# Kernel tuning notes

Hardware: AMD Instinct MI355X
Metric: run time of the kernel (lower is better)

Reference implementation:

```python
import jax, jax.numpy as jnp
import numpy as np

V = 32000        # vocab_size
OOV = 100        # max_oovs
VT = V + OOV
E = 256          # embed_size
H = 256          # hidden_size
PAD_INDEX = 0


def _gru_cell(x, h, w_ih, w_hh, b_ih, b_hh):
    # PyTorch GRU gate order: r, z, n
    gi = x @ w_ih.T + b_ih
    gh = h @ w_hh.T + b_hh
    ir, iz, inn = jnp.split(gi, 3, axis=-1)
    hr, hz, hn = jnp.split(gh, 3, axis=-1)
    r = jax.nn.sigmoid(ir + hr)
    z = jax.nn.sigmoid(iz + hz)
    n = jnp.tanh(inn + r * hn)
    return (1.0 - z) * n + z * h


def setup_inputs() -> dict:
    key = jax.random.key(0)
    ks = jax.random.split(key, 16)
    bs, max_len, seq_len = 32, 64, 128
    inputs = jax.random.randint(ks[0], (bs, max_len), 0, V, dtype=jnp.int32)
    encoded = jax.random.normal(ks[1], (bs, seq_len, 2 * H), dtype=jnp.float32)
    encoded_idx = jax.random.randint(ks[2], (bs, seq_len), 0, VT, dtype=jnp.int32)
    s = 0.02
    return {
        "inputs": inputs,
        "encoded": encoded,
        "encoded_idx": encoded_idx,
        "bridge_w": s * jax.random.normal(ks[3], (H, 2 * H), dtype=jnp.float32),
        "embed": s * jax.random.normal(ks[4], (V, E), dtype=jnp.float32),
        "gru_w_ih": s * jax.random.normal(ks[5], (3 * H, E + 2 * H), dtype=jnp.float32),
        "gru_w_hh": s * jax.random.normal(ks[6], (3 * H, H), dtype=jnp.float32),
        "gru_b_ih": jnp.zeros((3 * H,), dtype=jnp.float32),
        "gru_b_hh": jnp.zeros((3 * H,), dtype=jnp.float32),
        "Wg_w": s * jax.random.normal(ks[7], (V, H), dtype=jnp.float32),
        "Wg_b": jnp.zeros((V,), dtype=jnp.float32),
        "Wo_w": s * jax.random.normal(ks[8], (H, 2 * H), dtype=jnp.float32),
        "Wo_b": jnp.zeros((H,), dtype=jnp.float32),
    }


def decoder_forward(inputs, encoded, encoded_idx, bridge_w, embed,
                    gru_w_ih, gru_w_hh, gru_b_ih, gru_b_hh,
                    Wg_w, Wg_b, Wo_w, Wo_b):
    bs, seq_len, _ = encoded.shape
    # precomputed per-sequence quantities (as in original forward())
    enc_scores = jnp.tanh(encoded @ Wo_w.T + Wo_b)            # [bs, seq, H]
    pad_mask = jnp.where(encoded_idx == PAD_INDEX, -1000.0, 0.0)  # [bs, seq]
    b_idx = jnp.arange(bs)[:, None]

    s0 = encoded[:, -1, :] @ bridge_w.T                        # [bs, H]
    ctx0 = jnp.zeros((bs, 2 * H), dtype=encoded.dtype)

    def step(carry, inp):
        s_prev, ctx = carry
        x = embed[inp]                                         # [bs, E]
        gru_in = jnp.concatenate([x, ctx], axis=-1)            # [bs, E+2H]
        s_t = _gru_cell(gru_in, s_prev, gru_w_ih, gru_w_hh, gru_b_ih, gru_b_hh)
        psi_g = s_t @ Wg_w.T + Wg_b                            # [bs, V]
        psi_c = jnp.einsum('bsh,bh->bs', enc_scores, s_t) + pad_mask
        p = jax.nn.softmax(jnp.concatenate([psi_g, psi_c], axis=1), axis=1)
        prob_g = jnp.concatenate(
            [p[:, :V], jnp.full((bs, OOV), 1e-4, dtype=p.dtype)], axis=1)  # [bs, VT]
        prob_c = p[:, V:]                                      # [bs, seq]
        # scatter-add of copy probs onto extended vocab (one-hot bmm in original)
        prob_c_to_g = jnp.zeros((bs, VT), dtype=p.dtype).at[b_idx, encoded_idx].add(prob_c)
        out = prob_g + prob_c_to_g                             # [bs, VT]
        # selective read: reweight copy probs at positions matching current input
        rel = (encoded_idx == inp[:, None]).astype(p.dtype)
        cw = rel * prob_c
        cw = cw / jnp.maximum(cw.sum(axis=1, keepdims=True), 1e-12)  # F.normalize p=1
        new_ctx = jnp.einsum('bs,bsd->bd', cw, encoded)        # [bs, 2H]
        return (s_t, new_ctx), out

    (_, _), outs = jax.lax.scan(step, (s0, ctx0), inputs.T)    # [max_len, bs, VT]
    return jnp.transpose(outs, (1, 0, 2))                      # [bs, max_len, VT]


def reference(inputs, encoded, encoded_idx, bridge_w, embed,
              gru_w_ih, gru_w_hh, gru_b_ih, gru_b_hh,
              Wg_w, Wg_b, Wo_w, Wo_b):
    return decoder_forward(inputs, encoded, encoded_idx, bridge_w, embed,
                           gru_w_ih, gru_w_hh, gru_b_ih, gru_b_hh,
                           Wg_w, Wg_b, Wo_w, Wo_b)
```

## Files before the change

kernel.cpp:

```cpp
#include <hip/hip_runtime.h>
#include <math.h>
#include <stdint.h>

static const int VOC  = 32000;
static const int VT_  = 32100;

typedef __attribute__((ext_vector_type(8))) short bf16x8_t;
typedef __attribute__((ext_vector_type(4))) float f32x4_t;

__device__ __forceinline__ unsigned short f2bf(float f) {
  union { float f; unsigned int u; } v; v.f = f;
  unsigned int u = v.u;
  u = u + 0x7FFFu + ((u >> 16) & 1u);
  return (unsigned short)(u >> 16);
}
__device__ __forceinline__ float bf2f(unsigned short u) {
  union { unsigned int i; float f; } w; w.i = ((unsigned int)u) << 16; return w.f;
}
__device__ __forceinline__ float bfbits(unsigned int u) {
  union { unsigned int i; float f; } w; w.i = u; return w.f;
}
__device__ __forceinline__ int nth_set(unsigned long long m0, unsigned long long m1, int j) {
  int c0 = __popcll(m0);
  unsigned long long m = m0; int base = 0;
  if (j >= c0) { j -= c0; m = m1; base = 64; }
  for (int k = 0; k < j; k++) m &= m - 1;
  return base + (__ffsll((long long)m) - 1);
}

__global__ __launch_bounds__(256) void k_pre(
    const float* __restrict__ wg, unsigned short* __restrict__ WG16,
    const float* __restrict__ whh, unsigned short* __restrict__ WHH16,
    const float* __restrict__ enc, const float* __restrict__ wo,
    const float* __restrict__ wob, float* __restrict__ ENCSC,
    const float* __restrict__ bridge, float* __restrict__ S0,
    const float* __restrict__ embed, const int* __restrict__ inputs,
    const float* __restrict__ wih, const float* __restrict__ bih, float* __restrict__ XG,
    const int* __restrict__ encidx, float* __restrict__ ENCIH) {
  __shared__ int flag;
  int q = blockIdx.x;
  int tid = threadIdx.x;
  if (q < 256) {
    int bm = q >> 2, bn = q & 3;
    int ti = tid & 15, tj = tid >> 4;
    int r0 = bm * 64 + ti * 4;
    int n0 = bn * 64 + tj * 4;
    const float4* A[4]; const float4* B[4];
#pragma unroll
    for (int i = 0; i < 4; i++) A[i] = (const float4*)(enc + (size_t)(r0 + i) * 512);
#pragma unroll
    for (int j = 0; j < 4; j++) B[j] = (const float4*)(wo + (size_t)(n0 + j) * 512);
    float acc[4][4];
#pragma unroll
    for (int i = 0; i < 4; i++)
#pragma unroll
      for (int j = 0; j < 4; j++) acc[i][j] = 0.f;
    for (int k = 0; k < 128; k++) {
      float4 a[4], b[4];
#pragma unroll
      for (int i = 0; i < 4; i++) a[i] = A[i][k];
#pragma unroll
      for (int j = 0; j < 4; j++) b[j] = B[j][k];
#pragma unroll
      for (int i = 0; i < 4; i++)
#pragma unroll
        for (int j = 0; j < 4; j++)
          acc[i][j] += a[i].x * b[j].x + a[i].y * b[j].y + a[i].z * b[j].z + a[i].w * b[j].w;
    }
#pragma unroll
    for (int i = 0; i < 4; i++)
#pragma unroll
      for (int j = 0; j < 4; j++)
        ENCSC[(size_t)(r0 + i) * 256 + n0 + j] = tanhf(acc[i][j] + wob[n0 + j]);
  } else if (q < 640) {
    int p = q - 256;
    int bm = p & 31, bn = p >> 5;
    int ti = tid & 15, tj = tid >> 4;
    int r0 = bm * 64 + ti * 4;
    int n0 = bn * 64 + tj * 4;
    const float4* A[4]; const float4* B[4];
#pragma unroll
    for (int i = 0; i < 4; i++) A[i] = (const float4*)(embed + (size_t)inputs[r0 + i] * 256);
#pragma unroll
    for (int j = 0; j < 4; j++) B[j] = (const float4*)(wih + (size_t)(n0 + j) * 768);
    float acc[4][4];
#pragma unroll
    for (int i = 0; i < 4; i++)
#pragma unroll
      for (int j = 0; j < 4; j++) acc[i][j] = 0.f;
    for (int k = 0; k < 64; k++) {
      float4 a[4], b[4];
#pragma unroll
      for (int i = 0; i < 4; i++) a[i] = A[i][k];
#pragma unroll
      for (int j = 0; j < 4; j++) b[j] = B[j][k];
#pragma unroll
      for (int i = 0; i < 4; i++)
#pragma unroll
        for (int j = 0; j < 4; j++)
          acc[i][j] += a[i].x * b[j].x + a[i].y * b[j].y + a[i].z * b[j].z + a[i].w * b[j].w;
    }
#pragma unroll
    for (int i = 0; i < 4; i++)
#pragma unroll
      for (int j = 0; j < 4; j++)
        XG[(size_t)(r0 + i) * 768 + n0 + j] = acc[i][j] + bih[n0 + j];
  } else if (q < 1664) {
    int n4 = 32000 * 256 / 4;
    for (int i = (q - 640) * 256 + tid; i < n4; i += 1024 * 256) {
      float4 f = ((const float4*)wg)[i];
      ushort4 o;
      o.x = f2bf(f.x); o.y = f2bf(f.y); o.z = f2bf(f.z); o.w = f2bf(f.w);
      ((ushort4*)WG16)[i] = o;
    }
  } else if (q < 1676) {
    int n4 = 768 * 256 / 4;
    for (int i = (q - 1664) * 256 + tid; i < n4; i += 12 * 256) {
      float4 f = ((const float4*)whh)[i];
      ushort4 o;
      o.x = f2bf(f.x); o.y = f2bf(f.y); o.z = f2bf(f.z); o.w = f2bf(f.w);
      ((ushort4*)WHH16)[i] = o;
    }
  } else if (q < 1708) {
    int b = q - 1676, h = tid;
    const float4* a4 = (const float4*)(enc + ((size_t)b * 128 + 127) * 512);
    const float4* w4 = (const float4*)(bridge + (size_t)h * 512);
    float acc = 0.f;
    for (int k = 0; k < 128; k++) {
      float4 a = a4[k], w = w4[k];
      acc += a.x * w.x + a.y * w.y + a.z * w.z + a.w * w.w;
    }
    S0[b * 256 + h] = acc;
  } else {
    int bs = q - 1708;
    int b = bs >> 7;
    int idx = encidx[bs];
    if (tid < 64) {
      unsigned long long m = __ballot(inputs[b * 64 + tid] == idx);
      if (tid == 0) flag = (m != 0ULL);
    }
    __syncthreads();
    if (!flag) return;
    const float4* e4 = (const float4*)(enc + (size_t)bs * 512);
    for (int d = tid; d < 768; d += 256) {
      const float4* w4 = (const float4*)(wih + (size_t)d * 768 + 256);
      float acc = 0.f;
      for (int k = 0; k < 128; k++) {
        float4 e = e4[k], w = w4[k];
        acc += e.x * w.x + e.y * w.y + e.z * w.z + e.w * w.w;
      }
      ENCIH[(size_t)bs * 768 + d] = acc;
    }
  }
}

__global__ __launch_bounds__(768, 1) void k_seq(
    const unsigned short* __restrict__ whb,
    const float* __restrict__ bhh,
    const float* __restrict__ xg, const float* __restrict__ encsc,
    const float* __restrict__ encih, const int* __restrict__ encidx,
    const int* __restrict__ inputs, const float* __restrict__ s0,
    float* __restrict__ S32, unsigned short* __restrict__ S16) {
  __shared__ float sbuf[256];
  __shared__ __align__(16) unsigned short sb16[256];
  __shared__ float ghp[768];
  __shared__ float psis[128];
  __shared__ int eidx_sh[128];
  __shared__ int inp_sh[64];
  __shared__ unsigned long long mmask[64][2];
  __shared__ __align__(16) unsigned short wlds[73728];
  int b = blockIdx.x;
  int tid = threadIdx.x;
  int wid = tid >> 6, lane = tid & 63;
  int quad = lane >> 4, l15 = lane & 15;
  int n0 = wid * 64;
  int h = tid;
#pragma unroll
  for (int c = 0; c < 4; c++)
#pragma unroll
    for (int kt2 = 0; kt2 < 3; kt2++) {
      int4 v = *(const int4*)(whb + (size_t)(n0 + c * 16 + l15) * 256 + 160 + kt2 * 32 + quad * 8);
      *(int4*)(wlds + wid * 6144 + (c * 3 + kt2) * 512 + (l15 * 4 + quad) * 8) = v;
    }
  bf16x8_t wf[20];
#pragma unroll
  for (int c = 0; c < 4; c++)
#pragma unroll
    for (int kt = 0; kt < 5; kt++)
      wf[c * 5 + kt] = *(const bf16x8_t*)(whb + (size_t)(n0 + c * 16 + l15) * 256 + kt * 32 + quad * 8);
  float bR = 0.f, bZ = 0.f, bN = 0.f, ctxR = 0.f, ctxZ = 0.f, ctxN = 0.f;
  if (tid < 256) {
    bR = bhh[h]; bZ = bhh[256 + h]; bN = bhh[512 + h];
    float v = s0[b * 256 + tid];
    sbuf[tid] = v;
    sb16[tid] = f2bf(v);
  }
  if (tid < 128) eidx_sh[tid] = encidx[b * 128 + tid];
  if (tid < 64) inp_sh[tid] = inputs[b * 64 + tid];
  __syncthreads();
  if (tid < 128) {
    int e = eidx_sh[tid];
    for (int t = 0; t < 64; t++) {
      unsigned long long bal = __ballot(e == inp_sh[t]);
      if (lane == 0) mmask[t][wid] = bal;
    }
  }
  __syncthreads();
  for (int t = 0; t < 64; t++) {
    int r = b * 64 + t;
    float xr0 = 0.f, xr1 = 0.f, xr2 = 0.f;
    if (tid < 256) {
      const float* xr = xg + (size_t)r * 768;
      xr0 = xr[h]; xr1 = xr[256 + h]; xr2 = xr[512 + h];
    }
    f32x4_t a0 = {0.f,0.f,0.f,0.f}, a1 = {0.f,0.f,0.f,0.f};
    f32x4_t a2 = {0.f,0.f,0.f,0.f}, a3 = {0.f,0.f,0.f,0.f};
#pragma unroll
    for (int kt = 0; kt < 5; kt++) {
      bf16x8_t af = *(const bf16x8_t*)(sb16 + kt * 32 + quad * 8);
      a0 = __builtin_amdgcn_mfma_f32_16x16x32_bf16(af, wf[ 0 + kt], a0, 0, 0, 0);
      a1 = __builtin_amdgcn_mfma_f32_16x16x32_bf16(af, wf[ 5 + kt], a1, 0, 0, 0);
      a2 = __builtin_amdgcn_mfma_f32_16x16x32_bf16(af, wf[10 + kt], a2, 0, 0, 0);
      a3 = __builtin_amdgcn_mfma_f32_16x16x32_bf16(af, wf[15 + kt], a3, 0, 0, 0);
    }
#pragma unroll
    for (int kt2 = 0; kt2 < 3; kt2++) {
      bf16x8_t af = *(const bf16x8_t*)(sb16 + (5 + kt2) * 32 + quad * 8);
      const unsigned short* wb = wlds + wid * 6144 + kt2 * 512 + (l15 * 4 + quad) * 8;
      a0 = __builtin_amdgcn_mfma_f32_16x16x32_bf16(af, *(const bf16x8_t*)(wb +    0), a0, 0, 0, 0);
      a1 = __builtin_amdgcn_mfma_f32_16x16x32_bf16(af, *(const bf16x8_t*)(wb + 1536), a1, 0, 0, 0);
      a2 = __builtin_amdgcn_mfma_f32_16x16x32_bf16(af, *(const bf16x8_t*)(wb + 3072), a2, 0, 0, 0);
      a3 = __builtin_amdgcn_mfma_f32_16x16x32_bf16(af, *(const bf16x8_t*)(wb + 4608), a3, 0, 0, 0);
    }
    if (lane < 16) {
      ghp[n0 +      lane] = a0[0];
      ghp[n0 + 16 + lane] = a1[0];
      ghp[n0 + 32 + lane] = a2[0];
      ghp[n0 + 48 + lane] = a3[0];
    }
    __syncthreads();
    if (tid < 256) {
      float hr = ghp[h] + bR;
      float hz = ghp[256 + h] + bZ;
      float hn = ghp[512 + h] + bN;
      float gr = xr0 + ctxR;
      float gz = xr1 + ctxZ;
      float gn = xr2 + ctxN;
      float rgate = 1.f / (1.f + expf(-(gr + hr)));
      float zgate = 1.f / (1.f + expf(-(gz + hz)));
      float ngate = tanhf(gn + rgate * hn);
      float sold = sbuf[h];
      float snew = (1.f - zgate) * ngate + zgate * sold;
      unsigned short u16 = f2bf(snew);
      S32[(size_t)r * 256 + h] = snew;
      S16[(size_t)r * 256 + h] = u16;
      sbuf[h] = snew;
      sb16[h] = u16;
    }
    __syncthreads();
    if (t == 63) break;
    unsigned long long m0 = mmask[t][0], m1 = mmask[t][1];
    int mc = __popcll(m0) + __popcll(m1);
    if (mc > 0) {
      for (int j = wid; j < mc; j += 12) {
        int s = nth_set(m0, m1, j);
        const float4* e4 = (const float4*)(encsc + (size_t)(b * 128 + s) * 256);
        float4 ev = e4[lane];
        float4 sv = ((const float4*)sbuf)[lane];
        float v = ev.x * sv.x + ev.y * sv.y + ev.z * sv.z + ev.w * sv.w;
#pragma unroll
        for (int off = 32; off >= 1; off >>= 1) v += __shfl_down(v, off);
        if (lane == 0) psis[j] = v + (eidx_sh[s] == 0 ? -1000.f : 0.f);
      }
      __syncthreads();
      if (tid == 0) {
        float mx = -3e38f;
        for (int j = 0; j < mc; j++) mx = fmaxf(mx, psis[j]);
        if (mx < -500.f) {
          for (int j = 0; j < mc; j++) psis[j] = 0.f;
        } else {
          float ss = 0.f;
          for (int j = 0; j < mc; j++) { float e = expf(psis[j] - mx); psis[j] = e; ss += e; }
          float rs = 1.f / ss;
          for (int j = 0; j < mc; j++) psis[j] *= rs;
        }
      }
      __syncthreads();
      if (tid < 256) {
        ctxR = 0.f; ctxZ = 0.f; ctxN = 0.f;
        unsigned long long mm0 = m0, mm1 = m1;
        for (int j = 0; j < mc; j++) {
          int s;
          if (mm0) { s = __ffsll((long long)mm0) - 1; mm0 &= mm0 - 1; }
          else     { s = 64 + __ffsll((long long)mm1) - 1; mm1 &= mm1 - 1; }
          float c = psis[j];
          const float* e = encih + (size_t)(b * 128 + s) * 768;
          ctxR += c * e[h]; ctxZ += c * e[256 + h]; ctxN += c * e[512 + h];
        }
      }
    } else if (tid < 256) {
      ctxR = 0.f; ctxZ = 0.f; ctxN = 0.f;
    }
  }
}

__global__ __launch_bounds__(256, 2) void k_mid(const unsigned short* __restrict__ S16,
                                                const unsigned short* __restrict__ WG16,
                                                const float* __restrict__ wgb,
                                                unsigned short* __restrict__ pe16,
                                                const float* __restrict__ S32,
                                                const float* __restrict__ encsc,
                                                const int* __restrict__ encidx,
                                                float* __restrict__ psic) {
  __shared__ unsigned short lA[2][128 * 64];
  __shared__ unsigned short lB[2][128 * 64];
  int q = blockIdx.x;
  int tid = threadIdx.x;
  if (q >= 4000) {
    int q2 = q - 4000;
    int b = q2 >> 1, ny = q2 & 1;
    int ti = tid & 15, tj = tid >> 4;
    int r0 = b * 64 + ti * 4;
    int s0 = ny * 64 + tj * 4;
    const float4* A[4]; const float4* B[4];
#pragma unroll
    for (int i = 0; i < 4; i++) A[i] = (const float4*)(S32 + (size_t)(r0 + i) * 256);
#pragma unroll
    for (int j = 0; j < 4; j++) B[j] = (const float4*)(encsc + (size_t)(b * 128 + s0 + j) * 256);
    float acc[4][4];
#pragma unroll
    for (int i = 0; i < 4; i++)
#pragma unroll
      for (int j = 0; j < 4; j++) acc[i][j] = 0.f;
    for (int k = 0; k < 64; k++) {
      float4 a[4], bb[4];
#pragma unroll
      for (int i = 0; i < 4; i++) a[i] = A[i][k];
#pragma unroll
      for (int j = 0; j < 4; j++) bb[j] = B[j][k];
#pragma unroll
      for (int i = 0; i < 4; i++)
#pragma unroll
        for (int j = 0; j < 4; j++)
          acc[i][j] += a[i].x * bb[j].x + a[i].y * bb[j].y + a[i].z * bb[j].z + a[i].w * bb[j].w;
    }
#pragma unroll
    for (int i = 0; i < 4; i++)
#pragma unroll
      for (int j = 0; j < 4; j++) {
        float v = acc[i][j] + (encidx[b * 128 + s0 + j] == 0 ? -1000.f : 0.f);
        psic[(size_t)(r0 + i) * 128 + s0 + j] = v;
      }
    return;
  }
  int nc = q % 250, mt = q / 250;
  int wid = tid >> 6, lane = tid & 63;
  int wm = wid >> 1, wn = wid & 1;
  int quad = lane >> 4, l15 = lane & 15;
  f32x4_t acc[4][4];
#pragma unroll
  for (int i = 0; i < 4; i++)
#pragma unroll
    for (int j = 0; j < 4; j++) acc[i][j] = (f32x4_t){0.f, 0.f, 0.f, 0.f};

#define STAGE_MID(buf, kt) do {                                                            \
    _Pragma("unroll")                                                                      \
    for (int u = 0; u < 4; u++) {                                                          \
      int c = u * 256 + tid;                                                               \
      int row = c >> 3;                                                                    \
      int ko = ((c & 7) ^ (row & 7)) * 8;                                                  \
      __builtin_amdgcn_global_load_lds(                                                    \
          (const __attribute__((address_space(1))) unsigned int*)(S16 + (size_t)(mt * 128 + row) * 256 + (kt) * 64 + ko), \
          (__attribute__((address_space(3))) unsigned int*)(&lA[buf][c * 8]), 16, 0, 0);   \
      __builtin_amdgcn_global_load_lds(                                                    \
          (const __attribute__((address_space(1))) unsigned int*)(WG16 + (size_t)(nc * 128 + row) * 256 + (kt) * 64 + ko), \
          (__attribute__((address_space(3))) unsigned int*)(&lB[buf][c * 8]), 16, 0, 0);   \
    }                                                                                      \
  } while (0)

  STAGE_MID(0, 0);
  __syncthreads();
  for (int kt = 0; kt < 4; kt++) {
    int cur = kt & 1;
    if (kt < 3) STAGE_MID(cur ^ 1, kt + 1);
#pragma unroll
    for (int ks = 0; ks < 2; ks++) {
      bf16x8_t af[4], bfr[4];
      int slot = ((ks * 4 + quad) ^ (l15 & 7)) * 8;
#pragma unroll
      for (int i = 0; i < 4; i++) af[i] = *(const bf16x8_t*)(&lA[cur][(wm * 64 + i * 16 + l15) * 64 + slot]);
#pragma unroll
      for (int j = 0; j < 4; j++) bfr[j] = *(const bf16x8_t*)(&lB[cur][(wn * 64 + j * 16 + l15) * 64 + slot]);
#pragma unroll
      for (int i = 0; i < 4; i++)
#pragma unroll
        for (int j = 0; j < 4; j++)
          acc[i][j] = __builtin_amdgcn_mfma_f32_16x16x32_bf16(af[i], bfr[j], acc[i][j], 0, 0, 0);
    }
    __syncthreads();
  }
#undef STAGE_MID
  float bj[4];
#pragma unroll
  for (int j = 0; j < 4; j++) bj[j] = wgb[nc * 128 + wn * 64 + j * 16 + l15];
#pragma unroll
  for (int i = 0; i < 4; i++) {
#pragma unroll
    for (int p = 0; p < 4; p++) {
      int rg = mt * 128 + wm * 64 + i * 16 + quad * 4 + p;
      size_t base = (size_t)rg * 32000 + nc * 128 + wn * 64 + l15;
#pragma unroll
      for (int j = 0; j < 4; j++)
        pe16[base + j * 16] = f2bf(expf(acc[i][j][p] + bj[j]));
    }
  }
}

__global__ __launch_bounds__(256) void k_pb(const unsigned short* __restrict__ pe16,
                                            const float* __restrict__ psic,
                                            const int* __restrict__ encidx,
                                            float* __restrict__ outp) {
  __shared__ float red[8];
  int r = blockIdx.x;
  int b = r >> 6;
  int tid = threadIdx.x;
  int wid = tid >> 6, lane = tid & 63;
  const unsigned short* prow = pe16 + (size_t)r * 32000;
  float* orow = outp + (size_t)r * VT_;
  int4 ev[16];
#pragma unroll
  for (int u = 0; u < 16; u++) {
    int c8 = u * 256 + tid;
    if (c8 < 4000) ev[u] = *(const int4*)(prow + c8 * 8);
    else ev[u] = (int4){0, 0, 0, 0};
  }
  float sumE = 0.f;
#pragma unroll
  for (int u = 0; u < 16; u++) {
    unsigned int xs0 = (unsigned int)ev[u].x, xs1 = (unsigned int)ev[u].y;
    unsigned int xs2 = (unsigned int)ev[u].z, xs3 = (unsigned int)ev[u].w;
    sumE += bfbits(xs0 << 16) + bfbits(xs0 & 0xffff0000u);
    sumE += bfbits(xs1 << 16) + bfbits(xs1 & 0xffff0000u);
    sumE += bfbits(xs2 << 16) + bfbits(xs2 & 0xffff0000u);
    sumE += bfbits(xs3 << 16) + bfbits(xs3 & 0xffff0000u);
  }
  float t = sumE;
#pragma unroll
  for (int off = 32; off >= 1; off >>= 1) t += __shfl_xor(t, off);
  if (lane == 0) red[wid] = t;
  float pc = (tid < 128) ? psic[(size_t)r * 128 + tid] : -3e38f;
  float mv = pc;
#pragma unroll
  for (int off = 32; off >= 1; off >>= 1) mv = fmaxf(mv, __shfl_xor(mv, off));
  if (lane == 0) red[4 + wid] = mv;
  __syncthreads();
  float sumEt = red[0] + red[1] + red[2] + red[3];
  float Mc = fmaxf(fmaxf(red[4], red[5]), fmaxf(red[6], red[7]));
  float D = fmaxf(Mc - 30.f, 0.f);
  float w = expf(-D);
  __syncthreads();
  float ec = (tid < 128) ? expf(pc - D) : 0.f;
  float zt = ec;
#pragma unroll
  for (int off = 32; off >= 1; off >>= 1) zt += __shfl_xor(zt, off);
  if (lane == 0) red[wid] = zt;
  __syncthreads();
  float Z = w * sumEt + (red[0] + red[1] + red[2] + red[3]);
  float gs = w / Z;
#pragma unroll 2
  for (int u = 0; u < 16; u++) {
    int c8 = u * 256 + tid;
    if (c8 < 4000) {
      int c0 = c8 * 8;
      unsigned int xs0 = (unsigned int)ev[u].x, xs1 = (unsigned int)ev[u].y;
      unsigned int xs2 = (unsigned int)ev[u].z, xs3 = (unsigned int)ev[u].w;
      float4 o0, o1;
      o0.x = bfbits(xs0 << 16) * gs;         o0.y = bfbits(xs0 & 0xffff0000u) * gs;
      o0.z = bfbits(xs1 << 16) * gs;         o0.w = bfbits(xs1 & 0xffff0000u) * gs;
      o1.x = bfbits(xs2 << 16) * gs;         o1.y = bfbits(xs2 & 0xffff0000u) * gs;
      o1.z = bfbits(xs3 << 16) * gs;         o1.w = bfbits(xs3 & 0xffff0000u) * gs;
      *(float4*)(orow + c0) = o0;
      *(float4*)(orow + c0 + 4) = o1;
    }
  }
  if (tid < 100) orow[32000 + tid] = 1e-4f;
  __syncthreads();
  if (tid < 128) {
    int idx = encidx[b * 128 + tid];
    atomicAdd(&orow[idx], ec / Z);
  }
}

extern "C" void kernel_launch(void* const* d_in, const int* in_sizes, int n_in,
                              void* d_out, int out_size, void* d_ws, size_t ws_size,
                              hipStream_t stream) {
  (void)in_sizes; (void)n_in; (void)out_size; (void)ws_size;
  const int*   inputs  = (const int*)d_in[0];
  const float* encoded = (const float*)d_in[1];
  const int*   encidx  = (const int*)d_in[2];
  const float* bridge  = (const float*)d_in[3];
  const float* embed   = (const float*)d_in[4];
  const float* wih     = (const float*)d_in[5];
  const float* whh     = (const float*)d_in[6];
  const float* bih     = (const float*)d_in[7];
  const float* bhh     = (const float*)d_in[8];
  const float* wg      = (const float*)d_in[9];
  const float* wgb     = (const float*)d_in[10];
  const float* wo      = (const float*)d_in[11];
  const float* wob     = (const float*)d_in[12];
  float* out = (float*)d_out;

  char* ws = (char*)d_ws;
  size_t off = 0;
  auto alloc = [&](size_t bytes) -> void* {
    void* p = ws + off;
    off += (bytes + 255) & ~(size_t)255;
    return p;
  };
  unsigned short* WG16  = (unsigned short*)alloc((size_t)32000 * 256 * 2);
  unsigned short* WHH16 = (unsigned short*)alloc((size_t)768 * 256 * 2);
  float* S32            = (float*)alloc((size_t)2048 * 256 * 4);
  unsigned short* S16   = (unsigned short*)alloc((size_t)2048 * 256 * 2);
  float* ENCSC          = (float*)alloc((size_t)4096 * 256 * 4);
  float* ENCIH          = (float*)alloc((size_t)4096 * 768 * 4);
  float* XG             = (float*)alloc((size_t)2048 * 768 * 4);
  float* S0             = (float*)alloc((size_t)32 * 256 * 4);
  float* PSIC           = (float*)alloc((size_t)2048 * 128 * 4);
  unsigned short* PE16  = (unsigned short*)alloc((size_t)2048 * 32000 * 2);

  k_pre<<<5804, 256, 0, stream>>>(wg, WG16, whh, WHH16, encoded, wo, wob, ENCSC,
                                  bridge, S0, embed, inputs, wih, bih, XG,
                                  encidx, ENCIH);
  k_seq<<<32, 768, 0, stream>>>(WHH16, bhh, XG, ENCSC, ENCIH, encidx, inputs, S0, S32, S16);
  k_mid<<<4064, 256, 0, stream>>>(S16, WG16, wgb, PE16, S32, ENCSC, encidx, PSIC);
  k_pb<<<2048, 256, 0, stream>>>(PE16, PSIC, encidx, out);
}
```

Baseline: 837.0 us.

## Move precompute GEMMs to MFMA and make logits GEMM keep Wg tile resident

Splits the precompute kernel in two: the first converts enc/Wo into bf16 hi/lo pairs, and W_ih and the gathered embeddings into bf16. The second runs the encoder-score and input-gate GEMMs on MFMA, using a split-bf16 three-product scheme to keep fp32-like accuracy for the tanh scores. The logits kernel now launches one block per 128-column Wg tile, keeps the full-K tile in LDS, and loops over all 16 row tiles. This removes repeated Wg reloads at the cost of far fewer blocks (250), 128KB of LDS per block, and no double buffering.

```diff
diff --git a/kernel.cpp b/kernel.cpp
--- a/kernel.cpp
+++ b/kernel.cpp
@@ -28,101 +28,166 @@
   return base + (__ffsll((long long)m) - 1);
 }
 
-__global__ __launch_bounds__(256) void k_pre(
+__global__ __launch_bounds__(256) void k_pre0(
     const float* __restrict__ wg, unsigned short* __restrict__ WG16,
     const float* __restrict__ whh, unsigned short* __restrict__ WHH16,
-    const float* __restrict__ enc, const float* __restrict__ wo,
-    const float* __restrict__ wob, float* __restrict__ ENCSC,
-    const float* __restrict__ bridge, float* __restrict__ S0,
+    const float* __restrict__ enc, unsigned short* __restrict__ EH,
+    unsigned short* __restrict__ EL,
+    const float* __restrict__ wo, unsigned short* __restrict__ WOH,
+    unsigned short* __restrict__ WOL,
+    const float* __restrict__ wih, unsigned short* __restrict__ WIH16,
     const float* __restrict__ embed, const int* __restrict__ inputs,
-    const float* __restrict__ wih, const float* __restrict__ bih, float* __restrict__ XG,
-    const int* __restrict__ encidx, float* __restrict__ ENCIH) {
-  __shared__ int flag;
-  int q = blockIdx.x;
-  int tid = threadIdx.x;
-  if (q < 256) {
-    int bm = q >> 2, bn = q & 3;
-    int ti = tid & 15, tj = tid >> 4;
-    int r0 = bm * 64 + ti * 4;
-    int n0 = bn * 64 + tj * 4;
-    const float4* A[4]; const float4* B[4];
-#pragma unroll
-    for (int i = 0; i < 4; i++) A[i] = (const float4*)(enc + (size_t)(r0 + i) * 512);
-#pragma unroll
-    for (int j = 0; j < 4; j++) B[j] = (const float4*)(wo + (size_t)(n0 + j) * 512);
-    float acc[4][4];
-#pragma unroll
-    for (int i = 0; i < 4; i++)
-#pragma unroll
-      for (int j = 0; j < 4; j++) acc[i][j] = 0.f;
-    for (int k = 0; k < 128; k++) {
-      float4 a[4], b[4];
-#pragma unroll
-      for (int i = 0; i < 4; i++) a[i] = A[i][k];
-#pragma unroll
-      for (int j = 0; j < 4; j++) b[j] = B[j][k];
-#pragma unroll
-      for (int i = 0; i < 4; i++)
-#pragma unroll
-        for (int j = 0; j < 4; j++)
-          acc[i][j] += a[i].x * b[j].x + a[i].y * b[j].y + a[i].z * b[j].z + a[i].w * b[j].w;
-    }
-#pragma unroll
-    for (int i = 0; i < 4; i++)
-#pragma unroll
-      for (int j = 0; j < 4; j++)
-        ENCSC[(size_t)(r0 + i) * 256 + n0 + j] = tanhf(acc[i][j] + wob[n0 + j]);
-  } else if (q < 640) {
-    int p = q - 256;
-    int bm = p & 31, bn = p >> 5;
-    int ti = tid & 15, tj = tid >> 4;
-    int r0 = bm * 64 + ti * 4;
-    int n0 = bn * 64 + tj * 4;
-    const float4* A[4]; const float4* B[4];
-#pragma unroll
-    for (int i = 0; i < 4; i++) A[i] = (const float4*)(embed + (size_t)inputs[r0 + i] * 256);
-#pragma unroll
-    for (int j = 0; j < 4; j++) B[j] = (const float4*)(wih + (size_t)(n0 + j) * 768);
-    float acc[4][4];
-#pragma unroll
-    for (int i = 0; i < 4; i++)
-#pragma unroll
-      for (int j = 0; j < 4; j++) acc[i][j] = 0.f;
-    for (int k = 0; k < 64; k++) {
-      float4 a[4], b[4];
-#pragma unroll
-      for (int i = 0; i < 4; i++) a[i] = A[i][k];
-#pragma unroll
-      for (int j = 0; j < 4; j++) b[j] = B[j][k];
-#pragma unroll
-      for (int i = 0; i < 4; i++)
-#pragma unroll
-        for (int j = 0; j < 4; j++)
-          acc[i][j] += a[i].x * b[j].x + a[i].y * b[j].y + a[i].z * b[j].z + a[i].w * b[j].w;
-    }
-#pragma unroll
-    for (int i = 0; i < 4; i++)
-#pragma unroll
-      for (int j = 0; j < 4; j++)
-        XG[(size_t)(r0 + i) * 768 + n0 + j] = acc[i][j] + bih[n0 + j];
-  } else if (q < 1664) {
-    int n4 = 32000 * 256 / 4;
-    for (int i = (q - 640) * 256 + tid; i < n4; i += 1024 * 256) {
+    unsigned short* __restrict__ X16) {
+  int q = blockIdx.x, tid = threadIdx.x;
+  if (q < 1024) {
+    for (int i = q * 256 + tid; i < 2048000; i += 1024 * 256) {
       float4 f = ((const float4*)wg)[i];
       ushort4 o;
       o.x = f2bf(f.x); o.y = f2bf(f.y); o.z = f2bf(f.z); o.w = f2bf(f.w);
       ((ushort4*)WG16)[i] = o;
     }
-  } else if (q < 1676) {
-    int n4 = 768 * 256 / 4;
-    for (int i = (q - 1664) * 256 + tid; i < n4; i += 12 * 256) {
+  } else if (q < 1036) {
+    for (int i = (q - 1024) * 256 + tid; i < 49152; i += 12 * 256) {
       float4 f = ((const float4*)whh)[i];
       ushort4 o;
       o.x = f2bf(f.x); o.y = f2bf(f.y); o.z = f2bf(f.z); o.w = f2bf(f.w);
       ((ushort4*)WHH16)[i] = o;
     }
-  } else if (q < 1708) {
-    int b = q - 1676, h = tid;
+  } else if (q < 1292) {
+    for (int i = (q - 1036) * 256 + tid; i < 524288; i += 256 * 256) {
+      float4 f = ((const float4*)enc)[i];
+      ushort4 h, l;
+      h.x = f2bf(f.x); l.x = f2bf(f.x - bf2f(h.x));
+      h.y = f2bf(f.y); l.y = f2bf(f.y - bf2f(h.y));
+      h.z = f2bf(f.z); l.z = f2bf(f.z - bf2f(h.z));
+      h.w = f2bf(f.w); l.w = f2bf(f.w - bf2f(h.w));
+      ((ushort4*)EH)[i] = h;
+      ((ushort4*)EL)[i] = l;
+    }
+  } else if (q < 1300) {
+    for (int i = (q - 1292) * 256 + tid; i < 32768; i += 8 * 256) {
+      float4 f = ((const float4*)wo)[i];
+      ushort4 h, l;
+      h.x = f2bf(f.x); l.x = f2bf(f.x - bf2f(h.x));
+      h.y = f2bf(f.y); l.y = f2bf(f.y - bf2f(h.y));
+      h.z = f2bf(f.z); l.z = f2bf(f.z - bf2f(h.z));
+      h.w = f2bf(f.w); l.w = f2bf(f.w - bf2f(h.w));
+      ((ushort4*)WOH)[i] = h;
+      ((ushort4*)WOL)[i] = l;
+    }
+  } else if (q < 1312) {
+    for (int g = (q - 1300) * 256 + tid; g < 49152; g += 12 * 256) {
+      int row = g >> 6, col = g & 63;
+      float4 f = ((const float4*)(wih + (size_t)row * 768))[col];
+      ushort4 o;
+      o.x = f2bf(f.x); o.y = f2bf(f.y); o.z = f2bf(f.z); o.w = f2bf(f.w);
+      ((ushort4*)X16)[0];
+      ((ushort4*)WIH16)[g] = o;
+    }
+  } else {
+    for (int g = (q - 1312) * 256 + tid; g < 131072; g += 128 * 256) {
+      int r = g >> 6, col = g & 63;
+      float4 f = ((const float4*)(embed + (size_t)inputs[r] * 256))[col];
+      ushort4 o;
+      o.x = f2bf(f.x); o.y = f2bf(f.y); o.z = f2bf(f.z); o.w = f2bf(f.w);
+      ((ushort4*)X16)[g] = o;
+    }
+  }
+}
+
+__global__ __launch_bounds__(256) void k_pre1(
+    const unsigned short* __restrict__ EH, const unsigned short* __restrict__ EL,
+    const unsigned short* __restrict__ WOH, const unsigned short* __restrict__ WOL,
+    const float* __restrict__ wob, float* __restrict__ ENCSC,
+    const unsigned short* __restrict__ X16, const unsigned short* __restrict__ WIH16,
+    const float* __restrict__ bih, float* __restrict__ XG,
+    const float* __restrict__ enc, const float* __restrict__ bridge,
+    float* __restrict__ S0,
+    const float* __restrict__ wih, const int* __restrict__ encidx,
+    const int* __restrict__ inputs, float* __restrict__ ENCIH) {
+  __shared__ int flag;
+  int q = blockIdx.x, tid = threadIdx.x;
+  int wid = tid >> 6, lane = tid & 63;
+  int wm = wid >> 1, wn = wid & 1;
+  int quad = lane >> 4, l15 = lane & 15;
+  if (q < 256) {
+    int bm = q >> 2, bn = q & 3;
+    int r0 = bm * 64 + wm * 32, n0 = bn * 64 + wn * 32;
+    f32x4_t acc[2][2];
+#pragma unroll
+    for (int i = 0; i < 2; i++)
+#pragma unroll
+      for (int j = 0; j < 2; j++) acc[i][j] = (f32x4_t){0.f, 0.f, 0.f, 0.f};
+    for (int kc = 0; kc < 16; kc++) {
+      int ko = kc * 32 + quad * 8;
+      bf16x8_t ah[2], al[2], bh[2], bl[2];
+#pragma unroll
+      for (int i = 0; i < 2; i++) {
+        size_t off = (size_t)(r0 + i * 16 + l15) * 512 + ko;
+        ah[i] = *(const bf16x8_t*)(EH + off);
+        al[i] = *(const bf16x8_t*)(EL + off);
+      }
+#pragma unroll
+      for (int j = 0; j < 2; j++) {
+        size_t off = (size_t)(n0 + j * 16 + l15) * 512 + ko;
+        bh[j] = *(const bf16x8_t*)(WOH + off);
+        bl[j] = *(const bf16x8_t*)(WOL + off);
+      }
+#pragma unroll
+      for (int i = 0; i < 2; i++)
+#pragma unroll
+        for (int j = 0; j < 2; j++) {
+          acc[i][j] = __builtin_amdgcn_mfma_f32_16x16x32_bf16(ah[i], bh[j], acc[i][j], 0, 0, 0);
+          acc[i][j] = __builtin_amdgcn_mfma_f32_16x16x32_bf16(ah[i], bl[j], acc[i][j], 0, 0, 0);
+          acc[i][j] = __builtin_amdgcn_mfma_f32_16x16x32_bf16(al[i], bh[j], acc[i][j], 0, 0, 0);
+        }
+    }
+#pragma unroll
+    for (int i = 0; i < 2; i++)
+#pragma unroll
+      for (int j = 0; j < 2; j++)
+#pragma unroll
+        for (int p = 0; p < 4; p++) {
+          int row = r0 + i * 16 + quad * 4 + p;
+          int col = n0 + j * 16 + l15;
+          ENCSC[(size_t)row * 256 + col] = tanhf(acc[i][j][p] + wob[col]);
+        }
+  } else if (q < 640) {
+    int p2 = q - 256;
+    int bm = p2 & 31, bn = p2 >> 5;
+    int r0 = bm * 64 + wm * 32, n0 = bn * 64 + wn * 32;
+    f32x4_t acc[2][2];
+#pragma unroll
+    for (int i = 0; i < 2; i++)
+#pragma unroll
+      for (int j = 0; j < 2; j++) acc[i][j] = (f32x4_t){0.f, 0.f, 0.f, 0.f};
+    for (int kc = 0; kc < 8; kc++) {
+      int ko = kc * 32 + quad * 8;
+      bf16x8_t a[2], b[2];
+#pragma unroll
+      for (int i = 0; i < 2; i++)
+        a[i] = *(const bf16x8_t*)(X16 + (size_t)(r0 + i * 16 + l15) * 256 + ko);
+#pragma unroll
+      for (int j = 0; j < 2; j++)
+        b[j] = *(const bf16x8_t*)(WIH16 + (size_t)(n0 + j * 16 + l15) * 256 + ko);
+#pragma unroll
+      for (int i = 0; i < 2; i++)
+#pragma unroll
+        for (int j = 0; j < 2; j++)
+          acc[i][j] = __builtin_amdgcn_mfma_f32_16x16x32_bf16(a[i], b[j], acc[i][j], 0, 0, 0);
+    }
+#pragma unroll
+    for (int i = 0; i < 2; i++)
+#pragma unroll
+      for (int j = 0; j < 2; j++)
+#pragma unroll
+        for (int p = 0; p < 4; p++) {
+          int row = r0 + i * 16 + quad * 4 + p;
+          int col = n0 + j * 16 + l15;
+          XG[(size_t)row * 768 + col] = acc[i][j][p] + bih[col];
+        }
+  } else if (q < 672) {
+    int b = q - 640, h = tid;
     const float4* a4 = (const float4*)(enc + ((size_t)b * 128 + 127) * 512);
     const float4* w4 = (const float4*)(bridge + (size_t)h * 512);
     float acc = 0.f;
@@ -132,7 +197,7 @@
     }
     S0[b * 256 + h] = acc;
   } else {
-    int bs = q - 1708;
+    int bs = q - 672;
     int b = bs >> 7;
     int idx = encidx[bs];
     if (tid < 64) {
@@ -304,20 +369,18 @@
   }
 }
 
-__global__ __launch_bounds__(256, 2) void k_mid(const unsigned short* __restrict__ S16,
-                                                const unsigned short* __restrict__ WG16,
-                                                const float* __restrict__ wgb,
-                                                unsigned short* __restrict__ pe16,
-                                                const float* __restrict__ S32,
-                                                const float* __restrict__ encsc,
-                                                const int* __restrict__ encidx,
-                                                float* __restrict__ psic) {
-  __shared__ unsigned short lA[2][128 * 64];
-  __shared__ unsigned short lB[2][128 * 64];
+__global__ __launch_bounds__(256) void k_mid(const unsigned short* __restrict__ S16,
+                                             const unsigned short* __restrict__ WG16,
+                                             const float* __restrict__ wgb,
+                                             unsigned short* __restrict__ pe16,
+                                             const float* __restrict__ S32,
+                                             const float* __restrict__ encsc,
+                                             const int* __restrict__ encidx,
+                                             float* __restrict__ psic) {
   int q = blockIdx.x;
   int tid = threadIdx.x;
-  if (q >= 4000) {
-    int q2 = q - 4000;
+  if (q >= 250) {
+    int q2 = q - 250;
     int b = q2 >> 1, ny = q2 & 1;
     int ti = tid & 15, tj = tid >> 4;
     int r0 = b * 64 + ti * 4;
@@ -353,66 +416,68 @@
       }
     return;
   }
-  int nc = q % 250, mt = q / 250;
+  __shared__ unsigned short lB[128 * 256];
+  __shared__ unsigned short lA[128 * 256];
+  int nc = q;
   int wid = tid >> 6, lane = tid & 63;
   int wm = wid >> 1, wn = wid & 1;
   int quad = lane >> 4, l15 = lane & 15;
-  f32x4_t acc[4][4];
-#pragma unroll
-  for (int i = 0; i < 4; i++)
-#pragma unroll
-    for (int j = 0; j < 4; j++) acc[i][j] = (f32x4_t){0.f, 0.f, 0.f, 0.f};
-
-#define STAGE_MID(buf, kt) do {                                                            \
-    _Pragma("unroll")                                                                      \
-    for (int u = 0; u < 4; u++) {                                                          \
-      int c = u * 256 + tid;                                                               \
-      int row = c >> 3;                                                                    \
-      int ko = ((c & 7) ^ (row & 7)) * 8;                                                  \
-      __builtin_amdgcn_global_load_lds(                                                    \
-          (const __attribute__((address_space(1))) unsigned int*)(S16 + (size_t)(mt * 128 + row) * 256 + (kt) * 64 + ko), \
-          (__attribute__((address_space(3))) unsigned int*)(&lA[buf][c * 8]), 16, 0, 0);   \
-      __builtin_amdgcn_global_load_lds(                                                    \
-          (const __attribute__((address_space(1))) unsigned int*)(WG16 + (size_t)(nc * 128 + row) * 256 + (kt) * 64 + ko), \
-          (__attribute__((address_space(3))) unsigned int*)(&lB[buf][c * 8]), 16, 0, 0);   \
-    }                                                                                      \
-  } while (0)
-
-  STAGE_MID(0, 0);
-  __syncthreads();
-  for (int kt = 0; kt < 4; kt++) {
-    int cur = kt & 1;
-    if (kt < 3) STAGE_MID(cur ^ 1, kt + 1);
-#pragma unroll
-    for (int ks = 0; ks < 2; ks++) {
+#pragma unroll
+  for (int u = 0; u < 16; u++) {
+    int c = u * 256 + tid;
+    int row = c >> 5, ch = c & 31;
+    int sch = (ch & 24) | ((ch & 7) ^ (row & 7));
+    __builtin_amdgcn_global_load_lds(
+        (const __attribute__((address_space(1))) unsigned int*)(WG16 + (size_t)(nc * 128 + row) * 256 + sch * 8),
+        (__attribute__((address_space(3))) unsigned int*)(lB + c * 8), 16, 0, 0);
+  }
+  float bj[4];
+#pragma unroll
+  for (int j = 0; j < 4; j++) bj[j] = wgb[nc * 128 + wn * 64 + j * 16 + l15];
+  for (int mt = 0; mt < 16; mt++) {
+#pragma unroll
+    for (int u = 0; u < 16; u++) {
+      int c = u * 256 + tid;
+      int row = c >> 5, ch = c & 31;
+      int sch = (ch & 24) | ((ch & 7) ^ (row & 7));
+      __builtin_amdgcn_global_load_lds(
+          (const __attribute__((address_space(1))) unsigned int*)(S16 + (size_t)(mt * 128 + row) * 256 + sch * 8),
+          (__attribute__((address_space(3))) unsigned int*)(lA + c * 8), 16, 0, 0);
+    }
+    __syncthreads();
+    f32x4_t acc[4][4];
+#pragma unroll
+    for (int i = 0; i < 4; i++)
+#pragma unroll
+      for (int j = 0; j < 4; j++) acc[i][j] = (f32x4_t){0.f, 0.f, 0.f, 0.f};
+#pragma unroll
+    for (int kc = 0; kc < 8; kc++) {
+      int g = kc * 4 + quad;
+      int slotoff = ((g & 24) | ((g & 7) ^ (l15 & 7))) * 8;
       bf16x8_t af[4], bfr[4];
-      int slot = ((ks * 4 + quad) ^ (l15 & 7)) * 8;
-#pragma unroll
-      for (int i = 0; i < 4; i++) af[i] = *(const bf16x8_t*)(&lA[cur][(wm * 64 + i * 16 + l15) * 64 + slot]);
-#pragma unroll
-      for (int j = 0; j < 4; j++) bfr[j] = *(const bf16x8_t*)(&lB[cur][(wn * 64 + j * 16 + l15) * 64 + slot]);
+#pragma unroll
+      for (int i = 0; i < 4; i++)
+        af[i] = *(const bf16x8_t*)(lA + (wm * 64 + i * 16 + l15) * 256 + slotoff);
+#pragma unroll
+      for (int j = 0; j < 4; j++)
+        bfr[j] = *(const bf16x8_t*)(lB + (wn * 64 + j * 16 + l15) * 256 + slotoff);
 #pragma unroll
       for (int i = 0; i < 4; i++)
 #pragma unroll
         for (int j = 0; j < 4; j++)
           acc[i][j] = __builtin_amdgcn_mfma_f32_16x16x32_bf16(af[i], bfr[j], acc[i][j], 0, 0, 0);
     }
+#pragma unroll
+    for (int i = 0; i < 4; i++)
+#pragma unroll
+      for (int p = 0; p < 4; p++) {
+        int rg = mt * 128 + wm * 64 + i * 16 + quad * 4 + p;
+        size_t base = (size_t)rg * 32000 + nc * 128 + wn * 64 + l15;
+#pragma unroll
+        for (int j = 0; j < 4; j++)
+          pe16[base + j * 16] = f2bf(expf(acc[i][j][p] + bj[j]));
+      }
     __syncthreads();
-  }
-#undef STAGE_MID
-  float bj[4];
-#pragma unroll
-  for (int j = 0; j < 4; j++) bj[j] = wgb[nc * 128 + wn * 64 + j * 16 + l15];
-#pragma unroll
-  for (int i = 0; i < 4; i++) {
-#pragma unroll
-    for (int p = 0; p < 4; p++) {
-      int rg = mt * 128 + wm * 64 + i * 16 + quad * 4 + p;
-      size_t base = (size_t)rg * 32000 + nc * 128 + wn * 64 + l15;
-#pragma unroll
-      for (int j = 0; j < 4; j++)
-        pe16[base + j * 16] = f2bf(expf(acc[i][j][p] + bj[j]));
-    }
   }
 }
 
@@ -519,6 +584,12 @@
   };
   unsigned short* WG16  = (unsigned short*)alloc((size_t)32000 * 256 * 2);
   unsigned short* WHH16 = (unsigned short*)alloc((size_t)768 * 256 * 2);
+  unsigned short* EH    = (unsigned short*)alloc((size_t)4096 * 512 * 2);
+  unsigned short* EL    = (unsigned short*)alloc((size_t)4096 * 512 * 2);
+  unsigned short* WOH   = (unsigned short*)alloc((size_t)256 * 512 * 2);
+  unsigned short* WOL   = (unsigned short*)alloc((size_t)256 * 512 * 2);
+  unsigned short* WIH16 = (unsigned short*)alloc((size_t)768 * 256 * 2);
+  unsigned short* X16   = (unsigned short*)alloc((size_t)2048 * 256 * 2);
   float* S32            = (float*)alloc((size_t)2048 * 256 * 4);
   unsigned short* S16   = (unsigned short*)alloc((size_t)2048 * 256 * 2);
   float* ENCSC          = (float*)alloc((size_t)4096 * 256 * 4);
@@ -528,10 +599,12 @@
   float* PSIC           = (float*)alloc((size_t)2048 * 128 * 4);
   unsigned short* PE16  = (unsigned short*)alloc((size_t)2048 * 32000 * 2);
 
-  k_pre<<<5804, 256, 0, stream>>>(wg, WG16, whh, WHH16, encoded, wo, wob, ENCSC,
-                                  bridge, S0, embed, inputs, wih, bih, XG,
-                                  encidx, ENCIH);
+  k_pre0<<<1440, 256, 0, stream>>>(wg, WG16, whh, WHH16, encoded, EH, EL,
+                                   wo, WOH, WOL, wih, WIH16, embed, inputs, X16);
+  k_pre1<<<4768, 256, 0, stream>>>(EH, EL, WOH, WOL, wob, ENCSC,
+                                   X16, WIH16, bih, XG,
+                                   encoded, bridge, S0, wih, encidx, inputs, ENCIH);
   k_seq<<<32, 768, 0, stream>>>(WHH16, bhh, XG, ENCSC, ENCIH, encidx, inputs, S0, S32, S16);
-  k_mid<<<4064, 256, 0, stream>>>(S16, WG16, wgb, PE16, S32, ENCSC, encidx, PSIC);
+  k_mid<<<314, 256, 0, stream>>>(S16, WG16, wgb, PE16, S32, ENCSC, encidx, PSIC);
   k_pb<<<2048, 256, 0, stream>>>(PE16, PSIC, encidx, out);
 }
```

Result: faster. 776.2 us (-7.3%).
